# Kernel optimization log

Hardware: AMD Instinct MI355X
Metric: run time of the kernel (lower is better)

## Reference

```python
import jax, jax.numpy as jnp
import numpy as np

N_NODES = 100000
N_EDGES = 1600000
D_FEAT = 64


def setup_inputs() -> dict:
    key = jax.random.key(0)
    k1, k2, k3 = jax.random.split(key, 3)
    h = jax.random.normal(k1, (N_NODES, D_FEAT), dtype=jnp.float32)
    src = jax.random.randint(k2, (N_EDGES,), 0, N_NODES, dtype=jnp.int32)
    dst = jax.random.randint(k3, (N_EDGES,), 0, N_NODES, dtype=jnp.int32)
    edge_index = jnp.stack([src, dst], axis=0)  # [2, E]
    return {"h": h, "edge_index": edge_index}


def reference(h, edge_index):
    # EdgePassing: message = src node features (gather along edges)
    # Max_aggregation: per-dst-node max over incoming messages (segment max)
    src, dst = edge_index[0], edge_index[1]
    msgs = h[src]  # [E, D] gathered mailbox, never densified per-node
    agg = jax.ops.segment_max(msgs, dst, num_segments=N_NODES)  # [N, D]
    # DGL leaves nodes with no incoming messages at zero; segment_max yields -inf
    return jnp.where(jnp.isneginf(agg), jnp.zeros_like(agg), agg)
```

## Files before the change

kernel.cpp:

```cpp
#include <hip/hip_runtime.h>

#define D_FEAT 64
#define NEG_INF_BITS 0xFF800000u
#define ENC_NEG_INF  0x007FFFFFu
#define NPB 128
#define BSHIFT 7
#define BM_BLOCK 512
#define MAXB 1024

__device__ __forceinline__ unsigned enc_f32(float v) {
    unsigned b = __float_as_uint(v);
    return ((int)b >= 0) ? (b ^ 0x80000000u) : ~b;
}
__device__ __forceinline__ float dec_f32(unsigned u) {
    return (u & 0x80000000u) ? __uint_as_float(u ^ 0x80000000u) : __uint_as_float(~u);
}

__global__ void count_kernel(const int* __restrict__ dst, int* __restrict__ counts,
                             int E, int Te, int B) {
    __shared__ int lh[MAXB];
    for (int i = threadIdx.x; i < B; i += blockDim.x) lh[i] = 0;
    __syncthreads();
    int t = blockIdx.x;
    int beg = t * Te;
    int end = min(E, beg + Te);
    int nE = (end > beg) ? (end - beg) : 0;
    int n4 = nE >> 2;
    const int4* d4 = (const int4*)(dst + beg);
    for (int k = threadIdx.x; k < n4; k += blockDim.x) {
        int4 d = d4[k];
        atomicAdd(&lh[d.x >> BSHIFT], 1);
        atomicAdd(&lh[d.y >> BSHIFT], 1);
        atomicAdd(&lh[d.z >> BSHIFT], 1);
        atomicAdd(&lh[d.w >> BSHIFT], 1);
    }
    for (int i = beg + (n4 << 2) + threadIdx.x; i < end; i += blockDim.x)
        atomicAdd(&lh[dst[i] >> BSHIFT], 1);
    __syncthreads();
    for (int i = threadIdx.x; i < B; i += blockDim.x) counts[t * B + i] = lh[i];
}

__global__ void colscan_kernel(int* __restrict__ counts, int* __restrict__ hist,
                               int T, int B) {
    int w = (blockIdx.x * blockDim.x + threadIdx.x) >> 6;
    int lane = threadIdx.x & 63;
    if (w >= B) return;
    int b = w;
    int R = T >> 6;
    int v[4], pre[4];
    int base_t = lane * R;
    for (int r = 0; r < R; ++r) v[r] = counts[(base_t + r) * B + b];
    int s = 0;
    for (int r = 0; r < R; ++r) { pre[r] = s; s += v[r]; }
    int incl = s;
    for (int off = 1; off < 64; off <<= 1) {
        int tup = __shfl_up(incl, off);
        if (lane >= off) incl += tup;
    }
    int excl = incl - s;
    for (int r = 0; r < R; ++r) counts[(base_t + r) * B + b] = excl + pre[r];
    int total = __shfl(incl, 63);
    if (lane == 0) hist[b] = total;
}

__global__ void scan_kernel(const int* __restrict__ hist, int* __restrict__ bucket_start,
                            int B) {
    __shared__ int lds[MAXB];
    int tid = threadIdx.x;
    int v = (tid < B) ? hist[tid] : 0;
    lds[tid] = v;
    __syncthreads();
    for (int off = 1; off < MAXB; off <<= 1) {
        int t = (tid >= off) ? lds[tid - off] : 0;
        __syncthreads();
        lds[tid] += t;
        __syncthreads();
    }
    if (tid < B) {
        bucket_start[tid] = lds[tid] - v;
        if (tid == B - 1) bucket_start[B] = lds[tid];
    }
}

__global__ void place_kernel(const int* __restrict__ src, const int* __restrict__ dst,
                             const int* __restrict__ counts, const int* __restrict__ bucket_start,
                             unsigned* __restrict__ packed, int E, int Te, int B) {
    __shared__ int lcur[MAXB];
    int t = blockIdx.x;
    for (int i = threadIdx.x; i < B; i += blockDim.x)
        lcur[i] = bucket_start[i] + counts[t * B + i];
    __syncthreads();
    int beg = t * Te;
    int end = min(E, beg + Te);
    for (int i = beg + threadIdx.x; i < end; i += blockDim.x) {
        int d = dst[i];
        int b = d >> BSHIFT;
        int pos = atomicAdd(&lcur[b], 1);
        packed[pos] = (unsigned)src[i] | ((unsigned)(d & (NPB - 1)) << 17);
    }
}

__global__ void __launch_bounds__(BM_BLOCK)
bucket_max_kernel(const float* __restrict__ h,
                  const int* __restrict__ bucket_start,
                  const unsigned* __restrict__ packed,
                  float* __restrict__ out, int N) {
    __shared__ unsigned buf[NPB * D_FEAT];
    int b = blockIdx.x;
    int tid = threadIdx.x;
    int node0 = b << BSHIFT;
    int nvals = (min(NPB, N - node0)) * D_FEAT;

    for (int i = tid; i < NPB * D_FEAT; i += BM_BLOCK) buf[i] = ENC_NEG_INF;
    __syncthreads();

    int beg = bucket_start[b];
    int end = bucket_start[b + 1];
    int wid = tid >> 6;
    int lane = tid & 63;

    for (int base = beg + (wid << 6); base < end; base += BM_BLOCK) {
        int nk = min(64, end - base);
        unsigned p = (lane < nk) ? packed[base + lane] : 0u;
        int j = 0;
        for (; j + 8 <= nk; j += 8) {
            unsigned q[8];
            float v[8];
            #pragma unroll
            for (int k = 0; k < 8; ++k) q[k] = (unsigned)__shfl((int)p, j + k);
            #pragma unroll
            for (int k = 0; k < 8; ++k) v[k] = h[(q[k] & 0x1FFFFu) * D_FEAT + lane];
            #pragma unroll
            for (int k = 0; k < 8; ++k)
                atomicMax(&buf[(q[k] >> 17) * D_FEAT + lane], enc_f32(v[k]));
        }
        for (; j < nk; ++j) {
            unsigned pj = (unsigned)__shfl((int)p, j);
            float v = h[(pj & 0x1FFFFu) * D_FEAT + lane];
            atomicMax(&buf[(pj >> 17) * D_FEAT + lane], enc_f32(v));
        }
    }
    __syncthreads();

    for (int i = tid; i < nvals; i += BM_BLOCK) {
        unsigned u = buf[i];
        out[node0 * D_FEAT + i] = (u == ENC_NEG_INF) ? 0.0f : dec_f32(u);
    }
}

__global__ void init_out_kernel(uint4* __restrict__ out, int n4) {
    int i = blockIdx.x * blockDim.x + threadIdx.x;
    if (i < n4) {
        uint4 v;
        v.x = NEG_INF_BITS; v.y = NEG_INF_BITS; v.z = NEG_INF_BITS; v.w = NEG_INF_BITS;
        out[i] = v;
    }
}
__global__ void scatter_max_kernel(const float* __restrict__ h, const int* __restrict__ src,
                                   const int* __restrict__ dst, float* __restrict__ out, int E) {
    int gid = blockIdx.x * blockDim.x + threadIdx.x;
    int e = gid >> 6;
    if (e >= E) return;
    int lane = gid & 63;
    float v = h[src[e] * D_FEAT + lane];
    int* addr = (int*)(out + dst[e] * D_FEAT + lane);
    if (v >= 0.0f) atomicMax(addr, __float_as_int(v));
    else           atomicMin((unsigned int*)addr, __float_as_uint(v));
}
__global__ void finalize_kernel(float* __restrict__ out, int n) {
    int i = blockIdx.x * blockDim.x + threadIdx.x;
    if (i < n && __float_as_uint(out[i]) == NEG_INF_BITS) out[i] = 0.0f;
}

extern "C" void kernel_launch(void* const* d_in, const int* in_sizes, int n_in,
                              void* d_out, int out_size, void* d_ws, size_t ws_size,
                              hipStream_t stream) {
    const float* h = (const float*)d_in[0];
    const int* edge_index = (const int*)d_in[1];
    int E = in_sizes[1] / 2;
    const int* src = edge_index;
    const int* dst = edge_index + E;
    float* out = (float*)d_out;
    int N = out_size / D_FEAT;

    int B = (N + NPB - 1) >> BSHIFT;

    int T = 0;
    for (int cand = 256; cand >= 64; cand >>= 1) {
        size_t need = ((size_t)cand * B + B + (B + 1) + (size_t)E) * sizeof(int);
        if (ws_size >= need) { T = cand; break; }
    }

    if (N <= (1 << 17) && B <= MAXB && T > 0) {
        int* counts       = (int*)d_ws;
        int* hist         = counts + (size_t)T * B;
        int* bucket_start = hist + B;
        unsigned* packed  = (unsigned*)(bucket_start + B + 1);

        int Te = ((E + T - 1) / T + 3) & ~3;

        count_kernel<<<T, 512, 0, stream>>>(dst, counts, E, Te, B);
        int cs_blocks = (B * 64 + 511) / 512;
        colscan_kernel<<<cs_blocks, 512, 0, stream>>>(counts, hist, T, B);
        scan_kernel<<<1, MAXB, 0, stream>>>(hist, bucket_start, B);
        place_kernel<<<T, 512, 0, stream>>>(src, dst, counts, bucket_start, packed, E, Te, B);
        bucket_max_kernel<<<B, BM_BLOCK, 0, stream>>>(h, bucket_start, packed, out, N);
    } else {
        int n4 = out_size / 4;
        init_out_kernel<<<(n4 + 255) / 256, 256, 0, stream>>>((uint4*)out, n4);
        long long total = (long long)E * 64;
        scatter_max_kernel<<<(int)((total + 255) / 256), 256, 0, stream>>>(h, src, dst, out, E);
        finalize_kernel<<<(out_size + 255) / 256, 256, 0, stream>>>(out, out_size);
    }
}
```

Measured before the change: 164.0 us.

## Replace per-block count matrix with atomic bucket cursors and halve bucket size

```diff
diff --git a/kernel.cpp b/kernel.cpp
--- a/kernel.cpp
+++ b/kernel.cpp
@@ -1,12 +1,13 @@
 #include <hip/hip_runtime.h>
+#include <stdint.h>
 
 #define D_FEAT 64
 #define NEG_INF_BITS 0xFF800000u
 #define ENC_NEG_INF  0x007FFFFFu
-#define NPB 128
-#define BSHIFT 7
+#define NPB 64
+#define BSHIFT 6
 #define BM_BLOCK 512
-#define MAXB 1024
+#define MAXB 2048
 
 __device__ __forceinline__ unsigned enc_f32(float v) {
     unsigned b = __float_as_uint(v);
@@ -16,16 +17,65 @@
     return (u & 0x80000000u) ? __uint_as_float(u ^ 0x80000000u) : __uint_as_float(~u);
 }
 
-__global__ void count_kernel(const int* __restrict__ dst, int* __restrict__ counts,
-                             int E, int Te, int B) {
+__global__ void count_kernel(const int* __restrict__ dst, int* __restrict__ hist,
+                             int E, int B, int aligned4) {
     __shared__ int lh[MAXB];
     for (int i = threadIdx.x; i < B; i += blockDim.x) lh[i] = 0;
     __syncthreads();
+    int gid = blockIdx.x * blockDim.x + threadIdx.x;
+    int gstride = gridDim.x * blockDim.x;
+    int n4 = aligned4 ? (E >> 2) : 0;
+    const int4* d4 = (const int4*)dst;
+    for (int k = gid; k < n4; k += gstride) {
+        int4 d = d4[k];
+        atomicAdd(&lh[d.x >> BSHIFT], 1);
+        atomicAdd(&lh[d.y >> BSHIFT], 1);
+        atomicAdd(&lh[d.z >> BSHIFT], 1);
+        atomicAdd(&lh[d.w >> BSHIFT], 1);
+    }
+    for (int i = (n4 << 2) + gid; i < E; i += gstride)
+        atomicAdd(&lh[dst[i] >> BSHIFT], 1);
+    __syncthreads();
+    for (int i = threadIdx.x; i < B; i += blockDim.x) {
+        int c = lh[i];
+        if (c) atomicAdd(&hist[i], c);
+    }
+}
+
+__global__ void scan_kernel(const int* __restrict__ hist, int* __restrict__ bucket_start,
+                            int* __restrict__ cursor, int B) {
+    __shared__ int lds[MAXB / 2];
+    int tid = threadIdx.x;
+    int i0 = 2 * tid, i1 = 2 * tid + 1;
+    int v0 = (i0 < B) ? hist[i0] : 0;
+    int v1 = (i1 < B) ? hist[i1] : 0;
+    int s = v0 + v1;
+    lds[tid] = s;
+    __syncthreads();
+    for (int off = 1; off < (MAXB / 2); off <<= 1) {
+        int t = (tid >= off) ? lds[tid - off] : 0;
+        __syncthreads();
+        lds[tid] += t;
+        __syncthreads();
+    }
+    int excl = lds[tid] - s;
+    if (i0 < B) { bucket_start[i0] = excl;      cursor[i0] = excl; }
+    if (i1 < B) { bucket_start[i1] = excl + v0; cursor[i1] = excl + v0; }
+    if (tid == (MAXB / 2) - 1) bucket_start[B] = lds[tid];
+}
+
+__global__ void place_kernel(const int* __restrict__ src, const int* __restrict__ dst,
+                             int* __restrict__ cursor, unsigned* __restrict__ packed,
+                             int E, int Te, int B, int aligned4) {
+    __shared__ int lh[MAXB];
     int t = blockIdx.x;
     int beg = t * Te;
     int end = min(E, beg + Te);
-    int nE = (end > beg) ? (end - beg) : 0;
-    int n4 = nE >> 2;
+    if (beg >= end) return;
+    for (int i = threadIdx.x; i < B; i += blockDim.x) lh[i] = 0;
+    __syncthreads();
+    int nE = end - beg;
+    int n4 = aligned4 ? (nE >> 2) : 0;
     const int4* d4 = (const int4*)(dst + beg);
     for (int k = threadIdx.x; k < n4; k += blockDim.x) {
         int4 d = d4[k];
@@ -37,65 +87,15 @@
     for (int i = beg + (n4 << 2) + threadIdx.x; i < end; i += blockDim.x)
         atomicAdd(&lh[dst[i] >> BSHIFT], 1);
     __syncthreads();
-    for (int i = threadIdx.x; i < B; i += blockDim.x) counts[t * B + i] = lh[i];
-}
-
-__global__ void colscan_kernel(int* __restrict__ counts, int* __restrict__ hist,
-                               int T, int B) {
-    int w = (blockIdx.x * blockDim.x + threadIdx.x) >> 6;
-    int lane = threadIdx.x & 63;
-    if (w >= B) return;
-    int b = w;
-    int R = T >> 6;
-    int v[4], pre[4];
-    int base_t = lane * R;
-    for (int r = 0; r < R; ++r) v[r] = counts[(base_t + r) * B + b];
-    int s = 0;
-    for (int r = 0; r < R; ++r) { pre[r] = s; s += v[r]; }
-    int incl = s;
-    for (int off = 1; off < 64; off <<= 1) {
-        int tup = __shfl_up(incl, off);
-        if (lane >= off) incl += tup;
-    }
-    int excl = incl - s;
-    for (int r = 0; r < R; ++r) counts[(base_t + r) * B + b] = excl + pre[r];
-    int total = __shfl(incl, 63);
-    if (lane == 0) hist[b] = total;
-}
-
-__global__ void scan_kernel(const int* __restrict__ hist, int* __restrict__ bucket_start,
-                            int B) {
-    __shared__ int lds[MAXB];
-    int tid = threadIdx.x;
-    int v = (tid < B) ? hist[tid] : 0;
-    lds[tid] = v;
-    __syncthreads();
-    for (int off = 1; off < MAXB; off <<= 1) {
-        int t = (tid >= off) ? lds[tid - off] : 0;
-        __syncthreads();
-        lds[tid] += t;
-        __syncthreads();
-    }
-    if (tid < B) {
-        bucket_start[tid] = lds[tid] - v;
-        if (tid == B - 1) bucket_start[B] = lds[tid];
-    }
-}
-
-__global__ void place_kernel(const int* __restrict__ src, const int* __restrict__ dst,
-                             const int* __restrict__ counts, const int* __restrict__ bucket_start,
-                             unsigned* __restrict__ packed, int E, int Te, int B) {
-    __shared__ int lcur[MAXB];
-    int t = blockIdx.x;
-    for (int i = threadIdx.x; i < B; i += blockDim.x)
-        lcur[i] = bucket_start[i] + counts[t * B + i];
-    __syncthreads();
-    int beg = t * Te;
-    int end = min(E, beg + Te);
+    for (int i = threadIdx.x; i < B; i += blockDim.x) {
+        int c = lh[i];
+        lh[i] = c ? atomicAdd(&cursor[i], c) : 0;
+    }
+    __syncthreads();
     for (int i = beg + threadIdx.x; i < end; i += blockDim.x) {
         int d = dst[i];
         int b = d >> BSHIFT;
-        int pos = atomicAdd(&lcur[b], 1);
+        int pos = atomicAdd(&lh[b], 1);
         packed[pos] = (unsigned)src[i] | ((unsigned)(d & (NPB - 1)) << 17);
     }
 }
@@ -184,26 +184,23 @@
     int N = out_size / D_FEAT;
 
     int B = (N + NPB - 1) >> BSHIFT;
-
-    int T = 0;
-    for (int cand = 256; cand >= 64; cand >>= 1) {
-        size_t need = ((size_t)cand * B + B + (B + 1) + (size_t)E) * sizeof(int);
-        if (ws_size >= need) { T = cand; break; }
-    }
-
-    if (N <= (1 << 17) && B <= MAXB && T > 0) {
-        int* counts       = (int*)d_ws;
-        int* hist         = counts + (size_t)T * B;
+    size_t need = ((size_t)3 * B + 1 + (size_t)E) * sizeof(int);
+
+    if (N <= (1 << 17) && B <= MAXB && E > 0 && ws_size >= need) {
+        int* hist         = (int*)d_ws;
         int* bucket_start = hist + B;
-        unsigned* packed  = (unsigned*)(bucket_start + B + 1);
-
-        int Te = ((E + T - 1) / T + 3) & ~3;
-
-        count_kernel<<<T, 512, 0, stream>>>(dst, counts, E, Te, B);
-        int cs_blocks = (B * 64 + 511) / 512;
-        colscan_kernel<<<cs_blocks, 512, 0, stream>>>(counts, hist, T, B);
-        scan_kernel<<<1, MAXB, 0, stream>>>(hist, bucket_start, B);
-        place_kernel<<<T, 512, 0, stream>>>(src, dst, counts, bucket_start, packed, E, Te, B);
+        int* cursor       = bucket_start + B + 1;
+        unsigned* packed  = (unsigned*)(cursor + B);
+
+        int aligned4 = ((((uintptr_t)dst) & 15) == 0) ? 1 : 0;
+
+        hipMemsetAsync(hist, 0, (size_t)B * sizeof(int), stream);
+
+        count_kernel<<<256, 512, 0, stream>>>(dst, hist, E, B, aligned4);
+        scan_kernel<<<1, MAXB / 2, 0, stream>>>(hist, bucket_start, cursor, B);
+        int Te = ((E + 255) / 256 + 3) & ~3;
+        int pblocks = (E + Te - 1) / Te;
+        place_kernel<<<pblocks, 512, 0, stream>>>(src, dst, cursor, packed, E, Te, B, aligned4);
         bucket_max_kernel<<<B, BM_BLOCK, 0, stream>>>(h, bucket_start, packed, out, N);
     } else {
         int n4 = out_size / 4;
```

After: 176.6 us. +7.7%, slower.

## Halve node buckets to 64 per block and raise partition count for bucketed segment-max

Applied to the files above, without the earlier changes.

```diff
diff --git a/kernel.cpp b/kernel.cpp
--- a/kernel.cpp
+++ b/kernel.cpp
@@ -1,23 +1,25 @@
 #include <hip/hip_runtime.h>
+#include <stdint.h>
 
 #define D_FEAT 64
 #define NEG_INF_BITS 0xFF800000u
 #define ENC_NEG_INF  0x007FFFFFu
-#define NPB 128
-#define BSHIFT 7
-#define BM_BLOCK 512
-#define MAXB 1024
+#define NPB 64
+#define BSHIFT 6
+#define BM_BLOCK 256
+#define MAXB 2048
 
 __device__ __forceinline__ unsigned enc_f32(float v) {
     unsigned b = __float_as_uint(v);
     return ((int)b >= 0) ? (b ^ 0x80000000u) : ~b;
 }
-__device__ __forceinline__ float dec_f32(unsigned u) {
-    return (u & 0x80000000u) ? __uint_as_float(u ^ 0x80000000u) : __uint_as_float(~u);
+__device__ __forceinline__ unsigned dec_bits(unsigned u) {
+    if (u == ENC_NEG_INF) return 0u;
+    return (u & 0x80000000u) ? (u ^ 0x80000000u) : ~u;
 }
 
 __global__ void count_kernel(const int* __restrict__ dst, int* __restrict__ counts,
-                             int E, int Te, int B) {
+                             int E, int Te, int B, int aligned4) {
     __shared__ int lh[MAXB];
     for (int i = threadIdx.x; i < B; i += blockDim.x) lh[i] = 0;
     __syncthreads();
@@ -25,7 +27,7 @@
     int beg = t * Te;
     int end = min(E, beg + Te);
     int nE = (end > beg) ? (end - beg) : 0;
-    int n4 = nE >> 2;
+    int n4 = aligned4 ? (nE >> 2) : 0;
     const int4* d4 = (const int4*)(dst + beg);
     for (int k = threadIdx.x; k < n4; k += blockDim.x) {
         int4 d = d4[k];
@@ -42,44 +44,47 @@
 
 __global__ void colscan_kernel(int* __restrict__ counts, int* __restrict__ hist,
                                int T, int B) {
-    int w = (blockIdx.x * blockDim.x + threadIdx.x) >> 6;
-    int lane = threadIdx.x & 63;
-    if (w >= B) return;
-    int b = w;
-    int R = T >> 6;
-    int v[4], pre[4];
-    int base_t = lane * R;
-    for (int r = 0; r < R; ++r) v[r] = counts[(base_t + r) * B + b];
+    int b = blockIdx.x * blockDim.x + threadIdx.x;
+    if (b >= B) return;
     int s = 0;
-    for (int r = 0; r < R; ++r) { pre[r] = s; s += v[r]; }
-    int incl = s;
-    for (int off = 1; off < 64; off <<= 1) {
-        int tup = __shfl_up(incl, off);
-        if (lane >= off) incl += tup;
-    }
-    int excl = incl - s;
-    for (int r = 0; r < R; ++r) counts[(base_t + r) * B + b] = excl + pre[r];
-    int total = __shfl(incl, 63);
-    if (lane == 0) hist[b] = total;
+    int t = 0;
+    for (; t + 4 <= T; t += 4) {
+        int v0 = counts[(t + 0) * B + b];
+        int v1 = counts[(t + 1) * B + b];
+        int v2 = counts[(t + 2) * B + b];
+        int v3 = counts[(t + 3) * B + b];
+        counts[(t + 0) * B + b] = s; s += v0;
+        counts[(t + 1) * B + b] = s; s += v1;
+        counts[(t + 2) * B + b] = s; s += v2;
+        counts[(t + 3) * B + b] = s; s += v3;
+    }
+    for (; t < T; ++t) {
+        int v = counts[t * B + b];
+        counts[t * B + b] = s; s += v;
+    }
+    hist[b] = s;
 }
 
 __global__ void scan_kernel(const int* __restrict__ hist, int* __restrict__ bucket_start,
                             int B) {
-    __shared__ int lds[MAXB];
+    __shared__ int lds[MAXB / 2];
     int tid = threadIdx.x;
-    int v = (tid < B) ? hist[tid] : 0;
-    lds[tid] = v;
-    __syncthreads();
-    for (int off = 1; off < MAXB; off <<= 1) {
+    int i0 = 2 * tid, i1 = 2 * tid + 1;
+    int v0 = (i0 < B) ? hist[i0] : 0;
+    int v1 = (i1 < B) ? hist[i1] : 0;
+    int s = v0 + v1;
+    lds[tid] = s;
+    __syncthreads();
+    for (int off = 1; off < (MAXB / 2); off <<= 1) {
         int t = (tid >= off) ? lds[tid - off] : 0;
         __syncthreads();
         lds[tid] += t;
         __syncthreads();
     }
-    if (tid < B) {
-        bucket_start[tid] = lds[tid] - v;
-        if (tid == B - 1) bucket_start[B] = lds[tid];
-    }
+    int excl = lds[tid] - s;
+    if (i0 < B) bucket_start[i0] = excl;
+    if (i1 < B) bucket_start[i1] = excl + v0;
+    if (tid == (MAXB / 2) - 1) bucket_start[B] = lds[tid];
 }
 
 __global__ void place_kernel(const int* __restrict__ src, const int* __restrict__ dst,
@@ -142,9 +147,19 @@
     }
     __syncthreads();
 
-    for (int i = tid; i < nvals; i += BM_BLOCK) {
-        unsigned u = buf[i];
-        out[node0 * D_FEAT + i] = (u == ENC_NEG_INF) ? 0.0f : dec_f32(u);
+    if (nvals == NPB * D_FEAT) {
+        uint4* o4 = (uint4*)(out + (size_t)node0 * D_FEAT);
+        const uint4* b4 = (const uint4*)buf;
+        for (int i = tid; i < (NPB * D_FEAT) / 4; i += BM_BLOCK) {
+            uint4 u = b4[i];
+            uint4 r;
+            r.x = dec_bits(u.x); r.y = dec_bits(u.y);
+            r.z = dec_bits(u.z); r.w = dec_bits(u.w);
+            o4[i] = r;
+        }
+    } else {
+        unsigned* o = (unsigned*)(out + (size_t)node0 * D_FEAT);
+        for (int i = tid; i < nvals; i += BM_BLOCK) o[i] = dec_bits(buf[i]);
     }
 }
 
@@ -186,24 +201,25 @@
     int B = (N + NPB - 1) >> BSHIFT;
 
     int T = 0;
-    for (int cand = 256; cand >= 64; cand >>= 1) {
+    for (int cand = 1024; cand >= 64; cand >>= 1) {
         size_t need = ((size_t)cand * B + B + (B + 1) + (size_t)E) * sizeof(int);
         if (ws_size >= need) { T = cand; break; }
     }
 
-    if (N <= (1 << 17) && B <= MAXB && T > 0) {
+    if (N <= (1 << 17) && B <= MAXB && E > 0 && T > 0) {
         int* counts       = (int*)d_ws;
         int* hist         = counts + (size_t)T * B;
         int* bucket_start = hist + B;
         unsigned* packed  = (unsigned*)(bucket_start + B + 1);
 
         int Te = ((E + T - 1) / T + 3) & ~3;
-
-        count_kernel<<<T, 512, 0, stream>>>(dst, counts, E, Te, B);
-        int cs_blocks = (B * 64 + 511) / 512;
-        colscan_kernel<<<cs_blocks, 512, 0, stream>>>(counts, hist, T, B);
-        scan_kernel<<<1, MAXB, 0, stream>>>(hist, bucket_start, B);
-        place_kernel<<<T, 512, 0, stream>>>(src, dst, counts, bucket_start, packed, E, Te, B);
+        int aligned4 = ((((uintptr_t)dst) & 15) == 0) ? 1 : 0;
+
+        count_kernel<<<T, 256, 0, stream>>>(dst, counts, E, Te, B, aligned4);
+        int cs_blocks = (B + 255) / 256;
+        colscan_kernel<<<cs_blocks, 256, 0, stream>>>(counts, hist, T, B);
+        scan_kernel<<<1, MAXB / 2, 0, stream>>>(hist, bucket_start, B);
+        place_kernel<<<T, 256, 0, stream>>>(src, dst, counts, bucket_start, packed, E, Te, B);
         bucket_max_kernel<<<B, BM_BLOCK, 0, stream>>>(h, bucket_start, packed, out, N);
     } else {
         int n4 = out_size / 4;
```

Measured after the change: 250.9 us. +52.9%, slower.
